# Optimization experiments

Hardware: AMD Instinct MI355X
Metric: run time of the kernel (lower is better)

## Reference

```python
import jax, jax.numpy as jnp
import numpy as np

B, S, H = 1, 2048, 2048
NH, NKV, DH = 8, 1, 256
ROPE_THETA = 10000.0
SCALE = DH ** -0.5
NEG = -1e9


def setup_inputs() -> dict:
    key = jax.random.key(0)
    k1, k2, k3, k4, k5 = jax.random.split(key, 5)
    x = jax.random.normal(k1, (B, S, H), dtype=jnp.float32)
    position_ids = jnp.broadcast_to(jnp.arange(S, dtype=jnp.int32)[None, :], (B, S))
    causal = jnp.tril(jnp.ones((S, S), dtype=bool))
    attention_mask = jnp.where(causal, 0.0, NEG).astype(jnp.float32)[None, None]  # [1,1,S,S]
    std = 0.02
    w_q = jax.random.normal(k2, (H, NH * DH), dtype=jnp.float32) * std
    w_k = jax.random.normal(k3, (H, NKV * DH), dtype=jnp.float32) * std
    w_v = jax.random.normal(k4, (H, NKV * DH), dtype=jnp.float32) * std
    w_o = jax.random.normal(k5, (NH * DH, H), dtype=jnp.float32) * std
    return {"x": x, "position_ids": position_ids, "attention_mask": attention_mask,
            "w_q": w_q, "w_k": w_k, "w_v": w_v, "w_o": w_o}


def _rope_cos_sin(position_ids):
    # inv_freq: [DH/2]
    inv_freq = 1.0 / (ROPE_THETA ** (jnp.arange(0, DH, 2, dtype=jnp.float32) / DH))
    freqs = position_ids.astype(jnp.float32)[:, :, None] * inv_freq[None, None, :]  # [B,S,DH/2]
    emb = jnp.concatenate([freqs, freqs], axis=-1)  # [B,S,DH]
    return jnp.cos(emb), jnp.sin(emb)


def _rotate_half(t):
    t1, t2 = jnp.split(t, 2, axis=-1)
    return jnp.concatenate([-t2, t1], axis=-1)


def reference(x, position_ids, attention_mask, w_q, w_k, w_v, w_o):
    b, s, _ = x.shape
    g = NH // NKV  # kv group size
    q = (x @ w_q).reshape(b, s, NH, DH).transpose(0, 2, 1, 3)   # [b,nh,s,d]
    k = (x @ w_k).reshape(b, s, NKV, DH).transpose(0, 2, 1, 3)  # [b,nkv,s,d]
    v = (x @ w_v).reshape(b, s, NKV, DH).transpose(0, 2, 1, 3)
    cos, sin = _rope_cos_sin(position_ids)
    cos, sin = cos[:, None], sin[:, None]  # broadcast over heads
    q = q * cos + _rotate_half(q) * sin
    k = k * cos + _rotate_half(k) * sin
    # GQA: view q as [b,nkv,g,s,d]; equivalent to repeat_kv without materializing
    qg = q.reshape(b, NKV, g, s, DH)
    scores = jnp.einsum('bkgid,bkjd->bkgij', qg, k) * SCALE      # [b,nkv,g,s,s]
    scores = scores + attention_mask[:, :, None, :, :]
    attn = jax.nn.softmax(scores.astype(jnp.float32), axis=-1).astype(q.dtype)
    out = jnp.einsum('bkgij,bkjd->bkgid', attn, v)               # [b,nkv,g,s,d]
    out = out.reshape(b, NH, s, DH).transpose(0, 2, 1, 3).reshape(b, s, NH * DH)
    out = out @ w_o
    return out, attn.reshape(b, NH, s, s)
```

## Files before the change

kernel.cpp:

```cpp
#include <hip/hip_runtime.h>
#include <hip/hip_bf16.h>
#include <hip/hip_fp16.h>

typedef float f32x4 __attribute__((ext_vector_type(4)));
typedef _Float16 half8 __attribute__((ext_vector_type(8)));
typedef unsigned short u16;

#define DEVI __device__ __forceinline__

DEVI void async_cp16(void* lds, const void* g) {
  __builtin_amdgcn_global_load_lds(
      (const __attribute__((address_space(1))) void*)g,
      (__attribute__((address_space(3))) void*)lds,
      16, 0, 0);
}

DEVI u16 f2h(float x) {
  union { _Float16 h; u16 u; } v;
  v.h = (_Float16)x;
  return v.u;
}

__global__ __launch_bounds__(256)
void k_prep(const float* __restrict__ x, const float* __restrict__ wq,
            const float* __restrict__ wk, const float* __restrict__ wv,
            const float* __restrict__ wo,
            u16* __restrict__ xb, u16* __restrict__ wqkvT, u16* __restrict__ woT) {
  int bx = blockIdx.x;
  if (bx >= 72) {
    size_t base = ((size_t)(bx - 72) * 32 + blockIdx.y) * 2048 + threadIdx.x * 8;
    float4 v0 = *(const float4*)(x + base);
    float4 v1 = *(const float4*)(x + base + 4);
    ushort4 o0, o1;
    o0.x = f2h(v0.x); o0.y = f2h(v0.y); o0.z = f2h(v0.z); o0.w = f2h(v0.w);
    o1.x = f2h(v1.x); o1.y = f2h(v1.y); o1.z = f2h(v1.z); o1.w = f2h(v1.w);
    *(ushort4*)(xb + base) = o0;
    *(ushort4*)(xb + base + 4) = o1;
    return;
  }
  __shared__ u16 tile[64][65];
  const float* in; int ldin, rowoff, cx; u16* out;
  if (bx < 32)      { in = wq; ldin = 2048; out = wqkvT; rowoff = 0;    cx = bx; }
  else if (bx < 36) { in = wk; ldin = 256;  out = wqkvT; rowoff = 2048; cx = bx - 32; }
  else if (bx < 40) { in = wv; ldin = 256;  out = wqkvT; rowoff = 2304; cx = bx - 36; }
  else              { in = wo; ldin = 2048; out = woT;   rowoff = 0;    cx = bx - 40; }
  int r0 = blockIdx.y * 64, c0 = cx * 64;
  int tx = threadIdx.x & 63, ty = threadIdx.x >> 6;
  for (int rr = ty; rr < 64; rr += 4)
    tile[rr][tx] = f2h(in[(size_t)(r0 + rr) * ldin + (c0 + tx)]);
  __syncthreads();
  for (int rr = ty; rr < 64; rr += 4)
    out[(size_t)(c0 + rr + rowoff) * 2048 + (r0 + tx)] = tile[tx][rr];
}

__global__ __launch_bounds__(256)
void k_transpose2(const float* __restrict__ in0, const float* __restrict__ in1,
                  int ldin, u16* __restrict__ out, int ldout) {
  __shared__ u16 tile[64][65];
  int r0 = blockIdx.y * 64, c0 = blockIdx.x * 64;
  int tx = threadIdx.x & 63, ty = threadIdx.x >> 6;
  for (int rr = ty; rr < 64; rr += 4) {
    size_t idx = (size_t)(r0 + rr) * ldin + (c0 + tx);
    tile[rr][tx] = f2h(in0[idx] + in1[idx]);
  }
  __syncthreads();
  for (int rr = ty; rr < 64; rr += 4)
    out[(size_t)(c0 + rr) * ldout + (r0 + tx)] = tile[tx][rr];
}

__global__ __launch_bounds__(256)
void k_gemm128(const u16* __restrict__ A, int lda,
               const u16* __restrict__ B, int ldb,
               float* __restrict__ C0, float* __restrict__ C1,
               int ldc, int nmt, int Kloc) {
  const int bx = blockIdx.x;
  const int mt = bx % nmt, split = bx / nmt;
  float* __restrict__ C = split ? C1 : C0;
  const int i0 = mt * 128, j0 = blockIdx.y * 128;
  const size_t koff = (size_t)split * Kloc;

  __shared__ __align__(16) u16 As[2][128 * 32];
  __shared__ __align__(16) u16 Bs[2][128 * 32];
  const int tid = threadIdx.x;
  const int wave = tid >> 6, lane = tid & 63;
  const int wm = (wave >> 1) * 64, wn = (wave & 1) * 64;
  const int quad = lane >> 4, r = lane & 15;

  f32x4 acc[4][4] = {};

  const int ar = tid >> 2, ac = (tid & 3) * 8;
  const u16* ag0 = A + (size_t)(i0 + ar) * lda + ac + koff;
  const u16* ag1 = ag0 + (size_t)64 * lda;
  const u16* bg0 = B + (size_t)(j0 + ar) * ldb + ac + koff;
  const u16* bg1 = bg0 + (size_t)64 * ldb;
  const int l0 = tid * 8, l1 = (tid + 256) * 8;

  async_cp16(As[0] + l0, ag0); async_cp16(As[0] + l1, ag1);
  async_cp16(Bs[0] + l0, bg0); async_cp16(Bs[0] + l1, bg1);
  ag0 += 32; ag1 += 32; bg0 += 32; bg1 += 32;
  __syncthreads();

  const int nk = Kloc >> 5;
  for (int kt = 0; kt < nk; kt += 2) {
#pragma unroll
    for (int half = 0; half < 2; half++) {
      int cur = half, nxt = half ^ 1;
      if (kt + half + 1 < nk) {
        async_cp16(As[nxt] + l0, ag0); async_cp16(As[nxt] + l1, ag1);
        async_cp16(Bs[nxt] + l0, bg0); async_cp16(Bs[nxt] + l1, bg1);
        ag0 += 32; ag1 += 32; bg0 += 32; bg1 += 32;
      }
      half8 af[4], bf[4];
#pragma unroll
      for (int t = 0; t < 4; t++) af[t] = *(const half8*)(As[cur] + (wm + t * 16 + r) * 32 + quad * 8);
#pragma unroll
      for (int t = 0; t < 4; t++) bf[t] = *(const half8*)(Bs[cur] + (wn + t * 16 + r) * 32 + quad * 8);
#pragma unroll
      for (int ta = 0; ta < 4; ta++)
#pragma unroll
        for (int tb = 0; tb < 4; tb++)
          acc[ta][tb] = __builtin_amdgcn_mfma_f32_16x16x32_f16(af[ta], bf[tb], acc[ta][tb], 0, 0, 0);
      __syncthreads();
    }
  }
#pragma unroll
  for (int ta = 0; ta < 4; ta++) {
#pragma unroll
    for (int tb = 0; tb < 4; tb++) {
      int row = i0 + wm + ta * 16 + quad * 4;
      int col = j0 + wn + tb * 16 + r;
      float* cp = C + (size_t)row * ldc + col;
#pragma unroll
      for (int v = 0; v < 4; v++) cp[(size_t)v * ldc] = acc[ta][tb][v];
    }
  }
}

__global__ __launch_bounds__(256)
void k_add(float* __restrict__ dst, const float* __restrict__ src) {
  size_t idx = (size_t)blockIdx.x * 256 + threadIdx.x;
  float4 a = ((const float4*)dst)[idx];
  float4 b = ((const float4*)src)[idx];
  a.x += b.x; a.y += b.y; a.z += b.z; a.w += b.w;
  ((float4*)dst)[idx] = a;
}

__global__ __launch_bounds__(256)
void k_rope(const float* __restrict__ qkv0, const float* __restrict__ qkv1,
            const int* __restrict__ pos,
            u16* __restrict__ qh, u16* __restrict__ kh) {
  int idx = blockIdx.x * 256 + threadIdx.x;
  const int TOTAL_Q = 2048 * 1024;
  int s, i;
  size_t off;
  u16* dst;
  if (idx < TOTAL_Q) {
    s = idx >> 10;
    int hi = idx & 1023;
    int hd = hi >> 7;
    i = hi & 127;
    off = (size_t)s * 2560 + hd * 256;
    dst = qh + (size_t)s * 2048 + hd * 256;
  } else {
    int t = idx - TOTAL_Q;
    s = t >> 7;
    i = t & 127;
    off = (size_t)s * 2560 + 2048;
    dst = kh + (size_t)s * 256;
  }
  float p = (float)pos[s];
  float freq = __expf((float)i * (-9.210340371976184f / 128.0f)) * p;
  float sn, cs;
  sincosf(freq, &sn, &cs);
  float a = qkv0[off + i] + qkv1[off + i];
  float b = qkv0[off + i + 128] + qkv1[off + i + 128];
  dst[i]       = f2h(a * cs - b * sn);
  dst[i + 128] = f2h(b * cs + a * sn);
}

__global__ __launch_bounds__(256)
void k_scores(const u16* __restrict__ qh, const u16* __restrict__ kh,
              float* __restrict__ attn, float* __restrict__ lsum) {
  const int i0 = blockIdx.y * 128, j0 = blockIdx.x * 128;
  const int h = blockIdx.z;
  const int tid = threadIdx.x;
  float* outb = attn + ((size_t)h << 22);
  if (j0 > i0) {
    float4 z = {0.f, 0.f, 0.f, 0.f};
    int row = tid >> 5, col4 = (tid & 31) * 4;
    for (int s = 0; s < 16; s++)
      *(float4*)(outb + (size_t)(i0 + s * 8 + row) * 2048 + j0 + col4) = z;
    return;
  }
  const u16* A = qh + h * 256;
  __shared__ __align__(16) u16 As[2][128 * 32];
  __shared__ __align__(16) u16 Bs[2][128 * 32];
  __shared__ float psum[128];
  const int wave = tid >> 6, lane = tid & 63;
  const int wm = (wave >> 1) * 64, wn = (wave & 1) * 64;
  const int quad = lane >> 4, r = lane & 15;

  f32x4 acc[4][4] = {};

  const int ar = tid >> 2, ac = (tid & 3) * 8;
  const u16* ag0 = A + (size_t)(i0 + ar) * 2048 + ac;
  const u16* ag1 = ag0 + (size_t)64 * 2048;
  const u16* bg0 = kh + (size_t)(j0 + ar) * 256 + ac;
  const u16* bg1 = bg0 + (size_t)64 * 256;
  const int l0 = tid * 8, l1 = (tid + 256) * 8;

  async_cp16(As[0] + l0, ag0); async_cp16(As[0] + l1, ag1);
  async_cp16(Bs[0] + l0, bg0); async_cp16(Bs[0] + l1, bg1);
  ag0 += 32; ag1 += 32; bg0 += 32; bg1 += 32;
  __syncthreads();

  for (int kt = 0; kt < 8; kt += 2) {
#pragma unroll
    for (int half = 0; half < 2; half++) {
      int cur = half, nxt = half ^ 1;
      if (kt + half + 1 < 8) {
        async_cp16(As[nxt] + l0, ag0); async_cp16(As[nxt] + l1, ag1);
        async_cp16(Bs[nxt] + l0, bg0); async_cp16(Bs[nxt] + l1, bg1);
        ag0 += 32; ag1 += 32; bg0 += 32; bg1 += 32;
      }
      half8 af[4], bf[4];
#pragma unroll
      for (int t = 0; t < 4; t++) af[t] = *(const half8*)(As[cur] + (wm + t * 16 + r) * 32 + quad * 8);
#pragma unroll
      for (int t = 0; t < 4; t++) bf[t] = *(const half8*)(Bs[cur] + (wn + t * 16 + r) * 32 + quad * 8);
#pragma unroll
      for (int ta = 0; ta < 4; ta++)
#pragma unroll
        for (int tb = 0; tb < 4; tb++)
          acc[ta][tb] = __builtin_amdgcn_mfma_f32_16x16x32_f16(af[ta], bf[tb], acc[ta][tb], 0, 0, 0);
      __syncthreads();
    }
  }

  if (tid < 128) psum[tid] = 0.f;
  __syncthreads();
#pragma unroll
  for (int ta = 0; ta < 4; ta++) {
#pragma unroll
    for (int v = 0; v < 4; v++) {
      int row = i0 + wm + ta * 16 + quad * 4 + v;
      float rs = 0.f;
#pragma unroll
      for (int tb = 0; tb < 4; tb++) {
        int col = j0 + wn + tb * 16 + r;
        float val = (col <= row) ? __expf(acc[ta][tb][v] * 0.0625f) : 0.0f;
        outb[(size_t)row * 2048 + col] = val;
        rs += val;
      }
      rs += __shfl_xor(rs, 1); rs += __shfl_xor(rs, 2);
      rs += __shfl_xor(rs, 4); rs += __shfl_xor(rs, 8);
      if (r == 0) atomicAdd(&psum[wm + ta * 16 + quad * 4 + v], rs);
    }
  }
  __syncthreads();
  if (tid < 128)
    lsum[((size_t)h * 2048 + i0 + tid) * 16 + blockIdx.x] = psum[tid];
}

__global__ __launch_bounds__(256)
void k_pv(float* __restrict__ attn, const u16* __restrict__ vT,
          const float* __restrict__ lsum, u16* __restrict__ o) {
  const int h = blockIdx.y;
  const int i0 = blockIdx.x * 32;
  float* Ab = attn + ((size_t)h << 22);
  const int kmax = i0 + 32;
  __shared__ __align__(16) u16 As[32 * 32];
  __shared__ __align__(16) u16 Bs[256 * 32];
  __shared__ float inv_l[32];
  const int tid = threadIdx.x;
  const int wave = tid >> 6, lane = tid & 63;
  const int wn = wave * 64;
  const int quad = lane >> 4, r = lane & 15;

  if (tid < 32) {
    int i = i0 + tid;
    const float* lp = lsum + ((size_t)h * 2048 + i) * 16;
    int nt = (i >> 7) + 1;
    float s = 0.f;
    for (int t = 0; t < nt; t++) s += lp[t];
    inv_l[tid] = 1.0f / s;
  }
  __syncthreads();

  f32x4 acc[2][4] = {};
  const int br = tid >> 2, bc = (tid & 3) * 8;
  const u16* bg = vT + (size_t)br * 2048 + bc;
  const int arr = tid >> 3, ac4 = (tid & 7) * 4;
  float* agp = Ab + (size_t)(i0 + arr) * 2048 + ac4;
  const float ainv = inv_l[arr];

  for (int k0 = 0; k0 < kmax; k0 += 32) {
#pragma unroll
    for (int c = 0; c < 4; c++)
      async_cp16(Bs + tid * 8 + c * 2048, bg + (size_t)(c * 64) * 2048 + k0);
    float4 v = *(const float4*)(agp + k0);
    v.x *= ainv; v.y *= ainv; v.z *= ainv; v.w *= ainv;
    *(float4*)(agp + k0) = v;
    ushort4 w;
    w.x = f2h(v.x); w.y = f2h(v.y); w.z = f2h(v.z); w.w = f2h(v.w);
    *(ushort4*)(As + arr * 32 + ac4) = w;
    __syncthreads();
    half8 af[2], bf[4];
#pragma unroll
    for (int t = 0; t < 2; t++) af[t] = *(const half8*)(As + (t * 16 + r) * 32 + quad * 8);
#pragma unroll
    for (int t = 0; t < 4; t++) bf[t] = *(const half8*)(Bs + (wn + t * 16 + r) * 32 + quad * 8);
#pragma unroll
    for (int ta = 0; ta < 2; ta++)
#pragma unroll
      for (int tb = 0; tb < 4; tb++)
        acc[ta][tb] = __builtin_amdgcn_mfma_f32_16x16x32_f16(af[ta], bf[tb], acc[ta][tb], 0, 0, 0);
    __syncthreads();
  }
#pragma unroll
  for (int ta = 0; ta < 2; ta++) {
    int row = i0 + ta * 16 + quad * 4;
#pragma unroll
    for (int tb = 0; tb < 4; tb++) {
      int col = h * 256 + wn + tb * 16 + r;
#pragma unroll
      for (int v = 0; v < 4; v++)
        o[(size_t)(row + v) * 2048 + col] = f2h(acc[ta][tb][v]);
    }
  }
}

extern "C" void kernel_launch(void* const* d_in, const int* in_sizes, int n_in,
                              void* d_out, int out_size, void* d_ws, size_t ws_size,
                              hipStream_t stream) {
  const float* x   = (const float*)d_in[0];
  const int*   pos = (const int*)d_in[1];
  const float* w_q = (const float*)d_in[3];
  const float* w_k = (const float*)d_in[4];
  const float* w_v = (const float*)d_in[5];
  const float* w_o = (const float*)d_in[6];

  float* out  = (float*)d_out;
  float* attn = out + (size_t)2048 * 2048;

  char* ws = (char*)d_ws;
  float* qkv0  = (float*)ws;
  u16*   xb    = (u16*)(ws + (size_t)2048 * 2560 * 4);
  u16*   wqkvT = xb + (size_t)2048 * 2048;
  u16*   woT   = wqkvT + (size_t)2560 * 2048;
  u16*   qh    = woT + (size_t)2048 * 2048;
  u16*   kh    = qh + (size_t)2048 * 2048;
  u16*   vT    = kh + (size_t)2048 * 256;
  u16*   ob    = vT + (size_t)256 * 2048;
  float* lsum  = (float*)(ob + (size_t)2048 * 2048);

  float* qkv1  = attn;
  float* outp1 = (float*)xb;

  k_prep<<<dim3(136, 32), 256, 0, stream>>>(x, w_q, w_k, w_v, w_o, xb, wqkvT, woT);

  k_gemm128<<<dim3(32, 20), 256, 0, stream>>>(xb, 2048, wqkvT, 2048, qkv0, qkv1, 2560, 16, 1024);

  k_rope<<<(2048 * 1024 + 2048 * 128) / 256, 256, 0, stream>>>(qkv0, qkv1, pos, qh, kh);
  k_transpose2<<<dim3(4, 32), 256, 0, stream>>>(qkv0 + 2304, qkv1 + 2304, 2560, vT, 2048);

  k_scores<<<dim3(16, 16, 8), 256, 0, stream>>>(qh, kh, attn, lsum);
  k_pv<<<dim3(64, 8), 256, 0, stream>>>(attn, vT, lsum, ob);

  k_gemm128<<<dim3(32, 16), 256, 0, stream>>>(ob, 2048, woT, 2048, out, outp1, 2048, 16, 1024);
  k_add<<<4096, 256, 0, stream>>>(out, outp1);
}
```

Baseline: 385.7 us.

## Use 256x256 swizzled GEMM tiles, fuse V transpose into RoPE, pipeline PV

The projection GEMMs move to 256x256 tiles with 512 threads, BK=64, an XOR-swizzled LDS layout, XCD-aware block mapping and setprio around the MFMA bursts. The V transpose is folded into the RoPE kernel to save a launch. k_pv now double-buffers 64-wide K stages with swizzled LDS and issues the longest causal rows first. The aims are better operand reuse, fewer LDS bank conflicts and more overlap. The cost is much higher register and LDS pressure, and the GEMM grids shrink to 160 and 128 blocks, which may leave CUs idle.

```diff
diff --git a/kernel.cpp b/kernel.cpp
--- a/kernel.cpp
+++ b/kernel.cpp
@@ -5,6 +5,7 @@
 typedef float f32x4 __attribute__((ext_vector_type(4)));
 typedef _Float16 half8 __attribute__((ext_vector_type(8)));
 typedef unsigned short u16;
+typedef unsigned short u16x8 __attribute__((ext_vector_type(8)));
 
 #define DEVI __device__ __forceinline__
 
@@ -53,85 +54,90 @@
     out[(size_t)(c0 + rr + rowoff) * 2048 + (r0 + tx)] = tile[tx][rr];
 }
 
-__global__ __launch_bounds__(256)
-void k_transpose2(const float* __restrict__ in0, const float* __restrict__ in1,
-                  int ldin, u16* __restrict__ out, int ldout) {
-  __shared__ u16 tile[64][65];
-  int r0 = blockIdx.y * 64, c0 = blockIdx.x * 64;
-  int tx = threadIdx.x & 63, ty = threadIdx.x >> 6;
-  for (int rr = ty; rr < 64; rr += 4) {
-    size_t idx = (size_t)(r0 + rr) * ldin + (c0 + tx);
-    tile[rr][tx] = f2h(in0[idx] + in1[idx]);
-  }
-  __syncthreads();
-  for (int rr = ty; rr < 64; rr += 4)
-    out[(size_t)(c0 + rr) * ldout + (r0 + tx)] = tile[tx][rr];
-}
-
-__global__ __launch_bounds__(256)
-void k_gemm128(const u16* __restrict__ A, int lda,
+__global__ __launch_bounds__(512, 2)
+void k_gemm256(const u16* __restrict__ A, int lda,
                const u16* __restrict__ B, int ldb,
                float* __restrict__ C0, float* __restrict__ C1,
-               int ldc, int nmt, int Kloc) {
-  const int bx = blockIdx.x;
-  const int mt = bx % nmt, split = bx / nmt;
+               int ldc, int nN, int Kloc) {
+  const int id = blockIdx.x;
+  const int xcd = id & 7, t = id >> 3;
+  const int by = t % nN;
+  const int ms = xcd + 8 * (t / nN);
+  const int mt = ms & 7, split = ms >> 3;
   float* __restrict__ C = split ? C1 : C0;
-  const int i0 = mt * 128, j0 = blockIdx.y * 128;
+  const int i0 = mt * 256, j0 = by * 256;
   const size_t koff = (size_t)split * Kloc;
 
-  __shared__ __align__(16) u16 As[2][128 * 32];
-  __shared__ __align__(16) u16 Bs[2][128 * 32];
+  __shared__ __align__(16) u16 As[2][256 * 64];
+  __shared__ __align__(16) u16 Bs[2][256 * 64];
   const int tid = threadIdx.x;
   const int wave = tid >> 6, lane = tid & 63;
-  const int wm = (wave >> 1) * 64, wn = (wave & 1) * 64;
+  const int wm = (wave >> 2) * 128, wn = (wave & 3) * 64;
   const int quad = lane >> 4, r = lane & 15;
 
-  f32x4 acc[4][4] = {};
-
-  const int ar = tid >> 2, ac = (tid & 3) * 8;
-  const u16* ag0 = A + (size_t)(i0 + ar) * lda + ac + koff;
-  const u16* ag1 = ag0 + (size_t)64 * lda;
-  const u16* bg0 = B + (size_t)(j0 + ar) * ldb + ac + koff;
-  const u16* bg1 = bg0 + (size_t)64 * ldb;
-  const int l0 = tid * 8, l1 = (tid + 256) * 8;
-
-  async_cp16(As[0] + l0, ag0); async_cp16(As[0] + l1, ag1);
-  async_cp16(Bs[0] + l0, bg0); async_cp16(Bs[0] + l1, bg1);
-  ag0 += 32; ag1 += 32; bg0 += 32; bg1 += 32;
-  __syncthreads();
-
-  const int nk = Kloc >> 5;
-  for (int kt = 0; kt < nk; kt += 2) {
-#pragma unroll
-    for (int half = 0; half < 2; half++) {
-      int cur = half, nxt = half ^ 1;
-      if (kt + half + 1 < nk) {
-        async_cp16(As[nxt] + l0, ag0); async_cp16(As[nxt] + l1, ag1);
-        async_cp16(Bs[nxt] + l0, bg0); async_cp16(Bs[nxt] + l1, bg1);
-        ag0 += 32; ag1 += 32; bg0 += 32; bg1 += 32;
+  f32x4 acc[8][4] = {};
+
+  const int srow = tid >> 3;
+  const int scol = ((((tid & 7) << 4)) ^ ((srow & 7) << 4)) >> 1;
+  const u16* gA = A + (size_t)(i0 + srow) * lda + koff + scol;
+  const u16* gB = B + (size_t)(j0 + srow) * ldb + koff + scol;
+
+  const int cswz = (quad * 16) ^ ((r & 7) << 4);
+
+  const int nk = Kloc >> 6;
+
+#pragma unroll
+  for (int c = 0; c < 4; c++) {
+    async_cp16((u16*)As[0] + tid * 8 + c * 4096, gA + (size_t)(c * 64) * lda);
+    async_cp16((u16*)Bs[0] + tid * 8 + c * 4096, gB + (size_t)(c * 64) * ldb);
+  }
+
+  for (int kt = 0; kt < nk; kt++) {
+    const int cur = kt & 1;
+    __builtin_amdgcn_sched_barrier(0);
+    asm volatile("s_waitcnt vmcnt(0)" ::: "memory");
+    __builtin_amdgcn_s_barrier();
+    __builtin_amdgcn_sched_barrier(0);
+    if (kt + 1 < nk) {
+      const u16* a1 = gA + (size_t)(kt + 1) * 64;
+      const u16* b1 = gB + (size_t)(kt + 1) * 64;
+#pragma unroll
+      for (int c = 0; c < 4; c++) {
+        async_cp16((u16*)As[cur ^ 1] + tid * 8 + c * 4096, a1 + (size_t)(c * 64) * lda);
+        async_cp16((u16*)Bs[cur ^ 1] + tid * 8 + c * 4096, b1 + (size_t)(c * 64) * ldb);
       }
-      half8 af[4], bf[4];
-#pragma unroll
-      for (int t = 0; t < 4; t++) af[t] = *(const half8*)(As[cur] + (wm + t * 16 + r) * 32 + quad * 8);
-#pragma unroll
-      for (int t = 0; t < 4; t++) bf[t] = *(const half8*)(Bs[cur] + (wn + t * 16 + r) * 32 + quad * 8);
-#pragma unroll
-      for (int ta = 0; ta < 4; ta++)
-#pragma unroll
-        for (int tb = 0; tb < 4; tb++)
-          acc[ta][tb] = __builtin_amdgcn_mfma_f32_16x16x32_f16(af[ta], bf[tb], acc[ta][tb], 0, 0, 0);
-      __syncthreads();
-    }
-  }
-#pragma unroll
-  for (int ta = 0; ta < 4; ta++) {
-#pragma unroll
-    for (int tb = 0; tb < 4; tb++) {
-      int row = i0 + wm + ta * 16 + quad * 4;
-      int col = j0 + wn + tb * 16 + r;
+    }
+    const char* bufA = (const char*)As[cur];
+    const char* bufB = (const char*)Bs[cur];
+#pragma unroll
+    for (int kh = 0; kh < 2; kh++) {
+      const int inrow = cswz ^ (kh * 64);
+      half8 af[8], bf[4];
+#pragma unroll
+      for (int mm = 0; mm < 8; mm++)
+        af[mm] = *(const half8*)(bufA + (wm + mm * 16 + r) * 128 + inrow);
+#pragma unroll
+      for (int n = 0; n < 4; n++)
+        bf[n] = *(const half8*)(bufB + (wn + n * 16 + r) * 128 + inrow);
+      __builtin_amdgcn_s_setprio(1);
+#pragma unroll
+      for (int mm = 0; mm < 8; mm++)
+#pragma unroll
+        for (int n = 0; n < 4; n++)
+          acc[mm][n] = __builtin_amdgcn_mfma_f32_16x16x32_f16(af[mm], bf[n], acc[mm][n], 0, 0, 0);
+      __builtin_amdgcn_s_setprio(0);
+    }
+  }
+
+#pragma unroll
+  for (int mm = 0; mm < 8; mm++) {
+    int row = i0 + wm + mm * 16 + quad * 4;
+#pragma unroll
+    for (int n = 0; n < 4; n++) {
+      int col = j0 + wn + n * 16 + r;
       float* cp = C + (size_t)row * ldc + col;
 #pragma unroll
-      for (int v = 0; v < 4; v++) cp[(size_t)v * ldc] = acc[ta][tb][v];
+      for (int v = 0; v < 4; v++) cp[(size_t)v * ldc] = acc[mm][n][v];
     }
   }
 }
@@ -146,10 +152,25 @@
 }
 
 __global__ __launch_bounds__(256)
-void k_rope(const float* __restrict__ qkv0, const float* __restrict__ qkv1,
-            const int* __restrict__ pos,
-            u16* __restrict__ qh, u16* __restrict__ kh) {
-  int idx = blockIdx.x * 256 + threadIdx.x;
+void k_ropeT(const float* __restrict__ qkv0, const float* __restrict__ qkv1,
+             const int* __restrict__ pos,
+             u16* __restrict__ qh, u16* __restrict__ kh, u16* __restrict__ vT) {
+  __shared__ u16 tile[64][65];
+  int bx = blockIdx.x;
+  if (bx >= 9216) {
+    int b2 = bx - 9216;
+    int r0 = (b2 >> 2) * 64, c0 = (b2 & 3) * 64;
+    int tx = threadIdx.x & 63, ty = threadIdx.x >> 6;
+    for (int rr = ty; rr < 64; rr += 4) {
+      size_t idx = (size_t)(r0 + rr) * 2560 + 2304 + (c0 + tx);
+      tile[rr][tx] = f2h(qkv0[idx] + qkv1[idx]);
+    }
+    __syncthreads();
+    for (int rr = ty; rr < 64; rr += 4)
+      vT[(size_t)(c0 + rr) * 2048 + (r0 + tx)] = tile[tx][rr];
+    return;
+  }
+  int idx = bx * 256 + threadIdx.x;
   const int TOTAL_Q = 2048 * 1024;
   int s, i;
   size_t off;
@@ -266,11 +287,11 @@
 void k_pv(float* __restrict__ attn, const u16* __restrict__ vT,
           const float* __restrict__ lsum, u16* __restrict__ o) {
   const int h = blockIdx.y;
-  const int i0 = blockIdx.x * 32;
+  const int i0 = (63 - blockIdx.x) * 32;
   float* Ab = attn + ((size_t)h << 22);
   const int kmax = i0 + 32;
-  __shared__ __align__(16) u16 As[32 * 32];
-  __shared__ __align__(16) u16 Bs[256 * 32];
+  __shared__ __align__(16) u16 As[2][32 * 64];
+  __shared__ __align__(16) u16 Bs[2][256 * 64];
   __shared__ float inv_l[32];
   const int tid = threadIdx.x;
   const int wave = tid >> 6, lane = tid & 63;
@@ -287,35 +308,59 @@
   }
   __syncthreads();
 
+  const int arr = tid >> 3, ac8 = (tid & 7) * 8;
+  const int aso = arr * 64 + ((((tid & 7) * 16) ^ ((arr & 7) << 4)) >> 1);
+  float* agp = Ab + (size_t)(i0 + arr) * 2048 + ac8;
+  const float ainv = inv_l[arr];
+  const int brow = tid >> 3;
+  const int bcol = ((((tid & 7) * 16)) ^ (((tid >> 3) & 7) << 4)) >> 1;
+  const u16* bg = vT + (size_t)brow * 2048 + bcol;
+  const int cswz = (quad * 16) ^ ((r & 7) << 4);
+
   f32x4 acc[2][4] = {};
-  const int br = tid >> 2, bc = (tid & 3) * 8;
-  const u16* bg = vT + (size_t)br * 2048 + bc;
-  const int arr = tid >> 3, ac4 = (tid & 7) * 4;
-  float* agp = Ab + (size_t)(i0 + arr) * 2048 + ac4;
-  const float ainv = inv_l[arr];
-
-  for (int k0 = 0; k0 < kmax; k0 += 32) {
-#pragma unroll
-    for (int c = 0; c < 4; c++)
-      async_cp16(Bs + tid * 8 + c * 2048, bg + (size_t)(c * 64) * 2048 + k0);
-    float4 v = *(const float4*)(agp + k0);
-    v.x *= ainv; v.y *= ainv; v.z *= ainv; v.w *= ainv;
-    *(float4*)(agp + k0) = v;
-    ushort4 w;
-    w.x = f2h(v.x); w.y = f2h(v.y); w.z = f2h(v.z); w.w = f2h(v.w);
-    *(ushort4*)(As + arr * 32 + ac4) = w;
+
+#define PV_STAGE(buf, k0)                                                        \
+  {                                                                              \
+    _Pragma("unroll")                                                            \
+    for (int c = 0; c < 8; c++)                                                  \
+      async_cp16((u16*)Bs[buf] + tid * 8 + c * 2048,                             \
+                 bg + (size_t)(c * 32) * 2048 + (k0));                           \
+    float4 v0 = *(const float4*)(agp + (k0));                                    \
+    float4 v1 = *(const float4*)(agp + (k0) + 4);                                \
+    v0.x *= ainv; v0.y *= ainv; v0.z *= ainv; v0.w *= ainv;                      \
+    v1.x *= ainv; v1.y *= ainv; v1.z *= ainv; v1.w *= ainv;                      \
+    *(float4*)(agp + (k0)) = v0;                                                 \
+    *(float4*)(agp + (k0) + 4) = v1;                                             \
+    u16x8 w;                                                                     \
+    w[0] = f2h(v0.x); w[1] = f2h(v0.y); w[2] = f2h(v0.z); w[3] = f2h(v0.w);      \
+    w[4] = f2h(v1.x); w[5] = f2h(v1.y); w[6] = f2h(v1.z); w[7] = f2h(v1.w);      \
+    *(u16x8*)((u16*)As[buf] + aso) = w;                                          \
+  }
+
+  PV_STAGE(0, 0);
+  const int nkt = (kmax + 63) >> 6;
+  for (int kt = 0; kt < nkt; kt++) {
+    const int cur = kt & 1;
     __syncthreads();
-    half8 af[2], bf[4];
-#pragma unroll
-    for (int t = 0; t < 2; t++) af[t] = *(const half8*)(As + (t * 16 + r) * 32 + quad * 8);
-#pragma unroll
-    for (int t = 0; t < 4; t++) bf[t] = *(const half8*)(Bs + (wn + t * 16 + r) * 32 + quad * 8);
-#pragma unroll
-    for (int ta = 0; ta < 2; ta++)
+    if (kt + 1 < nkt) PV_STAGE(cur ^ 1, (kt + 1) * 64);
+    const char* bA = (const char*)As[cur];
+    const char* bB = (const char*)Bs[cur];
+#pragma unroll
+    for (int kh = 0; kh < 2; kh++) {
+      const int inrow = cswz ^ (kh * 64);
+      half8 af[2], bf[4];
+#pragma unroll
+      for (int ta = 0; ta < 2; ta++)
+        af[ta] = *(const half8*)(bA + (ta * 16 + r) * 128 + inrow);
 #pragma unroll
       for (int tb = 0; tb < 4; tb++)
-        acc[ta][tb] = __builtin_amdgcn_mfma_f32_16x16x32_f16(af[ta], bf[tb], acc[ta][tb], 0, 0, 0);
-    __syncthreads();
+        bf[tb] = *(const half8*)(bB + (wn + tb * 16 + r) * 128 + inrow);
+#pragma unroll
+      for (int ta = 0; ta < 2; ta++)
+#pragma unroll
+        for (int tb = 0; tb < 4; tb++)
+          acc[ta][tb] = __builtin_amdgcn_mfma_f32_16x16x32_f16(af[ta], bf[tb], acc[ta][tb], 0, 0, 0);
+    }
   }
 #pragma unroll
   for (int ta = 0; ta < 2; ta++) {
@@ -359,14 +404,13 @@
 
   k_prep<<<dim3(136, 32), 256, 0, stream>>>(x, w_q, w_k, w_v, w_o, xb, wqkvT, woT);
 
-  k_gemm128<<<dim3(32, 20), 256, 0, stream>>>(xb, 2048, wqkvT, 2048, qkv0, qkv1, 2560, 16, 1024);
-
-  k_rope<<<(2048 * 1024 + 2048 * 128) / 256, 256, 0, stream>>>(qkv0, qkv1, pos, qh, kh);
-  k_transpose2<<<dim3(4, 32), 256, 0, stream>>>(qkv0 + 2304, qkv1 + 2304, 2560, vT, 2048);
+  k_gemm256<<<dim3(160), 512, 0, stream>>>(xb, 2048, wqkvT, 2048, qkv0, qkv1, 2560, 10, 1024);
+
+  k_ropeT<<<9344, 256, 0, stream>>>(qkv0, qkv1, pos, qh, kh, vT);
 
   k_scores<<<dim3(16, 16, 8), 256, 0, stream>>>(qh, kh, attn, lsum);
   k_pv<<<dim3(64, 8), 256, 0, stream>>>(attn, vT, lsum, ob);
 
-  k_gemm128<<<dim3(32, 16), 256, 0, stream>>>(ob, 2048, woT, 2048, out, outp1, 2048, 16, 1024);
+  k_gemm256<<<dim3(128), 512, 0, stream>>>(ob, 2048, woT, 2048, out, outp1, 2048, 8, 1024);
   k_add<<<4096, 256, 0, stream>>>(out, outp1);
 }
```

After: 372.2 us. -3.5%, faster.
